# Kernel optimization log

Hardware: AMD Instinct MI355X
Metric: run time of the kernel (lower is better)

The kernel has to match this reference:

```python
import jax, jax.numpy as jnp
import numpy as np

TOP_K = 2
TEMP = 0.9
EPS = 1e-5
B, S, D, F, E = 2, 2048, 1024, 4096, 8


def setup_inputs() -> dict:
    key = jax.random.key(0)
    ks = jax.random.split(key, 4)
    scale_in = 1.0 / np.sqrt(D)
    scale_ff = 1.0 / np.sqrt(F)
    return {
        "x": jax.random.normal(ks[0], (B, S, D), jnp.float32),
        "gate_w": jax.random.normal(ks[1], (D, E), jnp.float32) * scale_in,
        "gate_b": jnp.zeros((E,), jnp.float32),
        "w1": jax.random.normal(ks[2], (E, D, F), jnp.float32) * scale_in,
        "b1": jnp.zeros((E, F), jnp.float32),
        "w2": jax.random.normal(ks[3], (E, F, D), jnp.float32) * scale_ff,
        "b2": jnp.zeros((E, D), jnp.float32),
        "ln_g": jnp.ones((D,), jnp.float32),
        "ln_b": jnp.zeros((D,), jnp.float32),
    }


def _moe_forward(x, gate_w, gate_b, w1, b1, w2, b2, ln_g, ln_b):
    # Gating: top-k masked softmax over experts
    logits = (x @ gate_w + gate_b) / TEMP                       # [B,S,E]
    topk_vals, topk_idx = jax.lax.top_k(logits, TOP_K)          # [B,S,K]
    keep = jax.nn.one_hot(topk_idx, E, dtype=jnp.bool_).any(-2)  # [B,S,E]
    masked = jnp.where(keep, logits, -jnp.inf)
    gate_probs = jax.nn.softmax(masked, axis=-1)                # [B,S,E]

    # Dense all-expert FFN (faithful to the naive original)
    h = jnp.einsum('bsd,edf->bsef', x, w1) + b1                 # [B,S,E,F]
    h = jax.nn.gelu(h, approximate=False)
    expert_out = jnp.einsum('bsef,efd->bsed', h, w2) + b2       # [B,S,E,D]

    out = jnp.einsum('bse,bsed->bsd', gate_probs, expert_out)   # combine

    # Post LayerNorm (dropout is identity in eval)
    mu = out.mean(-1, keepdims=True)
    var = out.var(-1, keepdims=True)
    out = (out - mu) / jnp.sqrt(var + EPS) * ln_g + ln_b
    return out


def reference(x, gate_w, gate_b, w1, b1, w2, b2, ln_g, ln_b):
    return _moe_forward(x, gate_w, gate_b, w1, b1, w2, b2, ln_g, ln_b)
```

## Files before the change

### kernel.cpp

```cpp
#include <hip/hip_runtime.h>
#include <stdint.h>
#include <stddef.h>

#define T_TOK 4096
#define DD    1024
#define FF    4096
#define EE    8
#define MAXROWS 9216
#define MAXTILES 72

typedef unsigned short u16;
typedef unsigned int   u32;
typedef short  sh8 __attribute__((ext_vector_type(8)));
typedef __bf16 bf8 __attribute__((ext_vector_type(8)));
typedef float  fl4 __attribute__((ext_vector_type(4)));

__device__ __forceinline__ u32 f2b_u(float f){
  u32 u = __float_as_uint(f);
  return (u + 0x7FFFu + ((u >> 16) & 1u)) >> 16;
}
__device__ __forceinline__ u16 f2b(float f){ return (u16)f2b_u(f); }
__device__ __forceinline__ u32 pack2(float a, float b){ return f2b_u(a) | (f2b_u(b) << 16); }

__device__ __forceinline__ void gl_lds16(const u16* g, u16* l){
  __builtin_amdgcn_global_load_lds(
      (const __attribute__((address_space(1))) u32*)(g),
      (__attribute__((address_space(3))) u32*)(l), 16, 0, 0);
}

__device__ __forceinline__ fl4 mfma16(sh8 a, sh8 b, fl4 c){
  return __builtin_amdgcn_mfma_f32_16x16x32_bf16(
      __builtin_bit_cast(bf8, a), __builtin_bit_cast(bf8, b), c, 0, 0, 0);
}

__device__ __forceinline__ float gelu_f(float x){
  float x2 = x * x;
  float t  = fmaf(0.07135481283f, x2, 1.5957691216f);
  float u  = x * t;
  float e  = __expf(-u);
  return x * __frcp_rn(1.0f + e);
}

__global__ __launch_bounds__(256) void k_cvt_x(const float* __restrict__ x,
                                               u16* __restrict__ xb){
  size_t i = ((size_t)blockIdx.x * 256 + threadIdx.x) * 8;
  float4 a = *(const float4*)(x + i);
  float4 b = *(const float4*)(x + i + 4);
  uint4 v;
  v.x = pack2(a.x, a.y); v.y = pack2(a.z, a.w);
  v.z = pack2(b.x, b.y); v.w = pack2(b.z, b.w);
  *(uint4*)(xb + i) = v;
}

__global__ __launch_bounds__(256) void k_gate(const float* __restrict__ x,
    const float* __restrict__ gw, const float* __restrict__ gb,
    int* __restrict__ tidx, float* __restrict__ tp, int* __restrict__ meta){
  int lane = threadIdx.x & 63;
  int t = blockIdx.x * 4 + (threadIdx.x >> 6);
  const float* xr = x + (size_t)t * DD;
  float a0=0,a1=0,a2=0,a3=0,a4=0,a5=0,a6=0,a7=0;
  #pragma unroll
  for (int i = 0; i < 16; i++){
    int d = i * 64 + lane;
    float xv = xr[d];
    const float4* g4 = (const float4*)(gw + (size_t)d * EE);
    float4 p = g4[0], q = g4[1];
    a0 += xv*p.x; a1 += xv*p.y; a2 += xv*p.z; a3 += xv*p.w;
    a4 += xv*q.x; a5 += xv*q.y; a6 += xv*q.z; a7 += xv*q.w;
  }
  #pragma unroll
  for (int off = 32; off > 0; off >>= 1){
    a0 += __shfl_xor(a0, off, 64); a1 += __shfl_xor(a1, off, 64);
    a2 += __shfl_xor(a2, off, 64); a3 += __shfl_xor(a3, off, 64);
    a4 += __shfl_xor(a4, off, 64); a5 += __shfl_xor(a5, off, 64);
    a6 += __shfl_xor(a6, off, 64); a7 += __shfl_xor(a7, off, 64);
  }
  if (lane == 0){
    float l[8] = {a0,a1,a2,a3,a4,a5,a6,a7};
    #pragma unroll
    for (int e = 0; e < 8; e++) l[e] = (l[e] + gb[e]) * (1.0f / 0.9f);
    int i1 = 0;
    #pragma unroll
    for (int e = 1; e < 8; e++) if (l[e] > l[i1]) i1 = e;
    int i2 = (i1 == 0) ? 1 : 0;
    #pragma unroll
    for (int e = 0; e < 8; e++) if (e != i1 && l[e] > l[i2]) i2 = e;
    float ex = expf(l[i2] - l[i1]);
    float inv = 1.0f / (1.0f + ex);
    tidx[2*t] = i1; tidx[2*t+1] = i2;
    tp[2*t] = inv;  tp[2*t+1] = ex * inv;
    atomicAdd(&meta[i1], 1);
    atomicAdd(&meta[i2], 1);
  }
}

__global__ __launch_bounds__(256) void k_fillscan(const int* __restrict__ tidx,
    const float* __restrict__ tp, int* __restrict__ meta,
    int* __restrict__ rowmap, float* __restrict__ rowp){
  __shared__ int sbase[EE];
  __shared__ int scur[EE];
  int tid = threadIdx.x;
  if (tid < EE) scur[tid] = 0;
  if (tid == 0){
    int rowbase = 0, total = 0;
    for (int e = 0; e < EE; e++){
      int c = meta[e];
      sbase[e] = rowbase;
      int nt = (c + 127) >> 7;
      for (int i = 0; i < nt; i++){
        meta[32 + total]  = e;
        meta[104 + total] = rowbase + i * 128;
        total++;
      }
      rowbase += nt << 7;
    }
    meta[24] = total;
  }
  __syncthreads();
  for (int t = tid; t < T_TOK; t += 256){
    #pragma unroll
    for (int k = 0; k < 2; k++){
      int e = tidx[2*t + k];
      int pos = atomicAdd(&scur[e], 1);
      int row = sbase[e] + pos;
      rowmap[row] = (t << 1) | k;
      rowp[row] = tp[2*t + k];
    }
  }
}

__global__ __launch_bounds__(256) void k_cvtw(const float* __restrict__ src,
    u16* __restrict__ dst, int R, int C){
  __shared__ float tile[64][65];
  int e = blockIdx.z;
  const float* se = src + (size_t)e * R * C;
  u16* de = dst + (size_t)e * R * C;
  int rblk = blockIdx.y * 64, cblk = blockIdx.x * 64;
  int tid = threadIdx.x;
  int lr = tid >> 4, lc = tid & 15;
  #pragma unroll
  for (int i = 0; i < 4; i++){
    int row = lr + i * 16;
    float4 v = *(const float4*)(se + (size_t)(rblk + row) * C + cblk + lc * 4);
    tile[row][lc*4+0] = v.x; tile[row][lc*4+1] = v.y;
    tile[row][lc*4+2] = v.z; tile[row][lc*4+3] = v.w;
  }
  __syncthreads();
  int c = tid >> 2, seg = tid & 3;
  u32 o[8];
  #pragma unroll
  for (int j = 0; j < 8; j++){
    float f0 = tile[seg*16 + 2*j    ][c];
    float f1 = tile[seg*16 + 2*j + 1][c];
    o[j] = pack2(f0, f1);
  }
  u16* dp = de + (size_t)(cblk + c) * R + rblk + seg * 16;
  *(uint4*)(dp)     = make_uint4(o[0], o[1], o[2], o[3]);
  *(uint4*)(dp + 8) = make_uint4(o[4], o[5], o[6], o[7]);
}

__global__ __launch_bounds__(256) void k_gemm_h(
    const u16* __restrict__ Xb, const u16* __restrict__ Wt,
    const float* __restrict__ b1, const int* __restrict__ meta,
    const int* __restrict__ rowmap, u16* __restrict__ H){
  __shared__ u16 As[128 * 64];
  __shared__ u16 Bs[128 * 64];
  int tx = blockIdx.x;
  if (tx >= meta[24]) return;
  int e = meta[32 + tx], row0 = meta[104 + tx];
  int n0 = blockIdx.y * 128;
  int tid = threadIdx.x;
  int rsub = tid >> 3;
  int sw_st = ((tid & 7) ^ (rsub & 7)) * 8;
  const u16* Be = Wt + ((size_t)e * FF + n0) * DD;
  const u16* gA[4];
  const u16* gB[4];
  #pragma unroll
  for (int j = 0; j < 4; j++){
    int row = j * 32 + rsub;
    int rm = rowmap[row0 + row];
    int tok = (rm < 0) ? 0 : (rm >> 1);
    gA[j] = Xb + (size_t)tok * DD + sw_st;
    gB[j] = Be + (size_t)row * DD + sw_st;
  }
  u16* lA = As + tid * 8;
  u16* lB = Bs + tid * 8;

  int lane = tid & 63, wv = tid >> 6;
  int wm = wv & 1, wn = wv >> 1;
  int lr = lane & 15, lq = lane >> 4;
  int sw0 = ((lq    ) ^ (lr & 7)) * 8;
  int sw1 = ((lq + 4) ^ (lr & 7)) * 8;
  const u16* pA = As + (wm * 64 + lr) * 64;
  const u16* pB = Bs + (wn * 64 + lr) * 64;

  fl4 acc[4][4];
  #pragma unroll
  for (int mi = 0; mi < 4; mi++)
    #pragma unroll
    for (int ni = 0; ni < 4; ni++) acc[mi][ni] = (fl4){0.f,0.f,0.f,0.f};

  for (int k0 = 0; k0 < DD; k0 += 64){
    #pragma unroll
    for (int j = 0; j < 4; j++){
      gl_lds16(gA[j] + k0, lA + j * 2048);
      gl_lds16(gB[j] + k0, lB + j * 2048);
    }
    __syncthreads();
    #pragma unroll
    for (int kk = 0; kk < 2; kk++){
      int sw = kk ? sw1 : sw0;
      sh8 a[4], b[4];
      #pragma unroll
      for (int mi = 0; mi < 4; mi++) a[mi] = *(const sh8*)(pA + mi * 1024 + sw);
      #pragma unroll
      for (int ni = 0; ni < 4; ni++) b[ni] = *(const sh8*)(pB + ni * 1024 + sw);
      #pragma unroll
      for (int mi = 0; mi < 4; mi++)
        #pragma unroll
        for (int ni = 0; ni < 4; ni++)
          acc[mi][ni] = mfma16(a[mi], b[ni], acc[mi][ni]);
    }
    __syncthreads();
  }

  const float* b1e = b1 + (size_t)e * FF;
  float bias[4];
  #pragma unroll
  for (int ni = 0; ni < 4; ni++) bias[ni] = b1e[n0 + wn*64 + ni*16 + lr];
  #pragma unroll
  for (int mi = 0; mi < 4; mi++){
    int grb = row0 + wm * 64 + mi * 16 + lq * 4;
    #pragma unroll
    for (int ni = 0; ni < 4; ni++){
      int gc = n0 + wn * 64 + ni * 16 + lr;
      #pragma unroll
      for (int r = 0; r < 4; r++){
        float v = acc[mi][ni][r] + bias[ni];
        H[(size_t)(grb + r) * FF + gc] = f2b(gelu_f(v));
      }
    }
  }
}

__global__ __launch_bounds__(256) void k_gemm_y(
    const u16* __restrict__ H, const u16* __restrict__ Wt,
    const float* __restrict__ b2, const int* __restrict__ meta,
    const int* __restrict__ rowmap, const float* __restrict__ rowp,
    float* __restrict__ slots){
  __shared__ u16 As[128 * 64];
  __shared__ u16 Bs[128 * 64];
  int tx = blockIdx.x;
  if (tx >= meta[24]) return;
  int e = meta[32 + tx], row0 = meta[104 + tx];
  int n0 = blockIdx.y * 128;
  int tid = threadIdx.x;
  int rsub = tid >> 3;
  int sw_st = ((tid & 7) ^ (rsub & 7)) * 8;
  const u16* Be = Wt + ((size_t)e * DD + n0) * FF;
  const u16* gA[4];
  const u16* gB[4];
  #pragma unroll
  for (int j = 0; j < 4; j++){
    int row = j * 32 + rsub;
    gA[j] = H + (size_t)(row0 + row) * FF + sw_st;
    gB[j] = Be + (size_t)row * FF + sw_st;
  }
  u16* lA = As + tid * 8;
  u16* lB = Bs + tid * 8;

  int lane = tid & 63, wv = tid >> 6;
  int wm = wv & 1, wn = wv >> 1;
  int lr = lane & 15, lq = lane >> 4;
  int sw0 = ((lq    ) ^ (lr & 7)) * 8;
  int sw1 = ((lq + 4) ^ (lr & 7)) * 8;
  const u16* pA = As + (wm * 64 + lr) * 64;
  const u16* pB = Bs + (wn * 64 + lr) * 64;

  fl4 acc[4][4];
  #pragma unroll
  for (int mi = 0; mi < 4; mi++)
    #pragma unroll
    for (int ni = 0; ni < 4; ni++) acc[mi][ni] = (fl4){0.f,0.f,0.f,0.f};

  for (int k0 = 0; k0 < FF; k0 += 64){
    #pragma unroll
    for (int j = 0; j < 4; j++){
      gl_lds16(gA[j] + k0, lA + j * 2048);
      gl_lds16(gB[j] + k0, lB + j * 2048);
    }
    __syncthreads();
    #pragma unroll
    for (int kk = 0; kk < 2; kk++){
      int sw = kk ? sw1 : sw0;
      sh8 a[4], b[4];
      #pragma unroll
      for (int mi = 0; mi < 4; mi++) a[mi] = *(const sh8*)(pA + mi * 1024 + sw);
      #pragma unroll
      for (int ni = 0; ni < 4; ni++) b[ni] = *(const sh8*)(pB + ni * 1024 + sw);
      #pragma unroll
      for (int mi = 0; mi < 4; mi++)
        #pragma unroll
        for (int ni = 0; ni < 4; ni++)
          acc[mi][ni] = mfma16(a[mi], b[ni], acc[mi][ni]);
    }
    __syncthreads();
  }

  const float* b2e = b2 + (size_t)e * DD;
  float bias[4];
  #pragma unroll
  for (int ni = 0; ni < 4; ni++) bias[ni] = b2e[n0 + wn*64 + ni*16 + lr];
  #pragma unroll
  for (int mi = 0; mi < 4; mi++){
    int grb = row0 + wm * 64 + mi * 16 + lq * 4;
    #pragma unroll
    for (int r = 0; r < 4; r++){
      int gr = grb + r;
      int sl = rowmap[gr];
      if (sl < 0) continue;
      float p = rowp[gr];
      #pragma unroll
      for (int ni = 0; ni < 4; ni++){
        int gc = n0 + wn * 64 + ni * 16 + lr;
        slots[(size_t)sl * DD + gc] = (acc[mi][ni][r] + bias[ni]) * p;
      }
    }
  }
}

__global__ __launch_bounds__(256) void k_ln(const float* __restrict__ slots,
    const float* __restrict__ lng, const float* __restrict__ lnb,
    float* __restrict__ out){
  int lane = threadIdx.x & 63;
  int t = blockIdx.x * 4 + (threadIdx.x >> 6);
  const float* s0 = slots + (size_t)(2 * t) * DD;
  const float* s1 = s0 + DD;
  float y[16];
  float sum = 0.f, sq = 0.f;
  #pragma unroll
  for (int i = 0; i < 2; i++){
    int d = lane * 8 + i * 512;
    float4 p0 = *(const float4*)(s0 + d);
    float4 p1 = *(const float4*)(s0 + d + 4);
    float4 q0 = *(const float4*)(s1 + d);
    float4 q1 = *(const float4*)(s1 + d + 4);
    y[i*8+0]=p0.x+q0.x; y[i*8+1]=p0.y+q0.y; y[i*8+2]=p0.z+q0.z; y[i*8+3]=p0.w+q0.w;
    y[i*8+4]=p1.x+q1.x; y[i*8+5]=p1.y+q1.y; y[i*8+6]=p1.z+q1.z; y[i*8+7]=p1.w+q1.w;
  }
  #pragma unroll
  for (int j = 0; j < 16; j++){ sum += y[j]; sq += y[j]*y[j]; }
  #pragma unroll
  for (int off = 32; off > 0; off >>= 1){
    sum += __shfl_xor(sum, off, 64);
    sq  += __shfl_xor(sq,  off, 64);
  }
  float mu = sum * (1.0f / DD);
  float var = sq * (1.0f / DD) - mu * mu;
  float rs = 1.0f / sqrtf(var + 1e-5f);
  #pragma unroll
  for (int i = 0; i < 2; i++){
    int d = lane * 8 + i * 512;
    float4 g0 = *(const float4*)(lng + d), g1 = *(const float4*)(lng + d + 4);
    float4 c0 = *(const float4*)(lnb + d), c1 = *(const float4*)(lnb + d + 4);
    float4 o0, o1;
    o0.x=(y[i*8+0]-mu)*rs*g0.x+c0.x; o0.y=(y[i*8+1]-mu)*rs*g0.y+c0.y;
    o0.z=(y[i*8+2]-mu)*rs*g0.z+c0.z; o0.w=(y[i*8+3]-mu)*rs*g0.w+c0.w;
    o1.x=(y[i*8+4]-mu)*rs*g1.x+c1.x; o1.y=(y[i*8+5]-mu)*rs*g1.y+c1.y;
    o1.z=(y[i*8+6]-mu)*rs*g1.z+c1.z; o1.w=(y[i*8+7]-mu)*rs*g1.w+c1.w;
    *(float4*)(out + (size_t)t * DD + d)     = o0;
    *(float4*)(out + (size_t)t * DD + d + 4) = o1;
  }
}

extern "C" void kernel_launch(void* const* d_in, const int* in_sizes, int n_in,
                              void* d_out, int out_size, void* d_ws, size_t ws_size,
                              hipStream_t stream){
  const float* x   = (const float*)d_in[0];
  const float* gw  = (const float*)d_in[1];
  const float* gb  = (const float*)d_in[2];
  const float* w1  = (const float*)d_in[3];
  const float* b1  = (const float*)d_in[4];
  const float* w2  = (const float*)d_in[5];
  const float* b2  = (const float*)d_in[6];
  const float* lng = (const float*)d_in[7];
  const float* lnb = (const float*)d_in[8];
  float* out = (float*)d_out;

  char* ws = (char*)d_ws;
  size_t off = 0;
  auto alloc = [&](size_t bytes) -> void* {
    void* p = ws + off;
    off = (off + bytes + 255) & ~(size_t)255;
    return p;
  };
  int*   meta   = (int*)  alloc(256 * 4);
  int*   rowmap = (int*)  alloc(MAXROWS * 4);
  float* rowp   = (float*)alloc(MAXROWS * 4);
  int*   tidx   = (int*)  alloc(2 * T_TOK * 4);
  float* tp     = (float*)alloc(2 * T_TOK * 4);
  u16*   Xb     = (u16*)  alloc((size_t)T_TOK * DD * 2);
  float* slots  = (float*)alloc((size_t)T_TOK * 2 * DD * 4);
  u16*   H      = (u16*)  alloc((size_t)MAXROWS * FF * 2);
  u16*   Wt     = (u16*)  alloc((size_t)EE * DD * FF * 2);
  (void)ws_size; (void)in_sizes; (void)n_in; (void)out_size;

  hipMemsetAsync(meta, 0, 64, stream);
  hipMemsetAsync(rowmap, 0xFF, MAXROWS * 4, stream);

  k_cvt_x   <<<(T_TOK * DD) / (256 * 8), 256, 0, stream>>>(x, Xb);
  k_gate    <<<T_TOK / 4, 256, 0, stream>>>(x, gw, gb, tidx, tp, meta);
  k_fillscan<<<1, 256, 0, stream>>>(tidx, tp, meta, rowmap, rowp);

  k_cvtw  <<<dim3(FF / 64, DD / 64, EE), 256, 0, stream>>>(w1, Wt, DD, FF);
  k_gemm_h<<<dim3(MAXTILES, FF / 128), 256, 0, stream>>>(Xb, Wt, b1, meta, rowmap, H);
  k_cvtw  <<<dim3(DD / 64, FF / 64, EE), 256, 0, stream>>>(w2, Wt, FF, DD);
  k_gemm_y<<<dim3(MAXTILES, DD / 128), 256, 0, stream>>>(H, Wt, b2, meta, rowmap, rowp, slots);

  k_ln    <<<T_TOK / 4, 256, 0, stream>>>(slots, lng, lnb, out);
}
```

Before: 709.8 us.

## Double-buffer LDS in both expert GEMMs and split-K the second GEMM

Both grouped GEMM kernels now use two LDS buffers, so the next K slice is loaded while MFMAs run on the current one, hiding global-load latency behind compute. The down-projection GEMM is also split along K into two halves across grid z. Partial results are combined with atomicAdd into a zero-initialised slots buffer, with the bias added only by the first half. This doubles the block count of the under-occupied second GEMM, at the cost of twice the LDS per block (64KB), an extra memset, and atomic traffic.

```diff
diff --git a/kernel.cpp b/kernel.cpp
--- a/kernel.cpp
+++ b/kernel.cpp
@@ -163,8 +163,7 @@
     const u16* __restrict__ Xb, const u16* __restrict__ Wt,
     const float* __restrict__ b1, const int* __restrict__ meta,
     const int* __restrict__ rowmap, u16* __restrict__ H){
-  __shared__ u16 As[128 * 64];
-  __shared__ u16 Bs[128 * 64];
+  __shared__ u16 A0[128*64], B0[128*64], A1[128*64], B1[128*64];
   int tx = blockIdx.x;
   if (tx >= meta[24]) return;
   int e = meta[32 + tx], row0 = meta[104 + tx];
@@ -183,16 +182,14 @@
     gA[j] = Xb + (size_t)tok * DD + sw_st;
     gB[j] = Be + (size_t)row * DD + sw_st;
   }
-  u16* lA = As + tid * 8;
-  u16* lB = Bs + tid * 8;
 
   int lane = tid & 63, wv = tid >> 6;
   int wm = wv & 1, wn = wv >> 1;
   int lr = lane & 15, lq = lane >> 4;
   int sw0 = ((lq    ) ^ (lr & 7)) * 8;
   int sw1 = ((lq + 4) ^ (lr & 7)) * 8;
-  const u16* pA = As + (wm * 64 + lr) * 64;
-  const u16* pB = Bs + (wn * 64 + lr) * 64;
+  int offA = (wm * 64 + lr) * 64;
+  int offB = (wn * 64 + lr) * 64;
 
   fl4 acc[4][4];
   #pragma unroll
@@ -200,28 +197,38 @@
     #pragma unroll
     for (int ni = 0; ni < 4; ni++) acc[mi][ni] = (fl4){0.f,0.f,0.f,0.f};
 
-  for (int k0 = 0; k0 < DD; k0 += 64){
+  auto stage = [&](int k0, u16* dA, u16* dB){
     #pragma unroll
     for (int j = 0; j < 4; j++){
-      gl_lds16(gA[j] + k0, lA + j * 2048);
-      gl_lds16(gB[j] + k0, lB + j * 2048);
-    }
-    __syncthreads();
+      gl_lds16(gA[j] + k0, dA + tid * 8 + j * 2048);
+      gl_lds16(gB[j] + k0, dB + tid * 8 + j * 2048);
+    }
+  };
+  auto compute = [&](const u16* bufA, const u16* bufB){
     #pragma unroll
     for (int kk = 0; kk < 2; kk++){
       int sw = kk ? sw1 : sw0;
       sh8 a[4], b[4];
       #pragma unroll
-      for (int mi = 0; mi < 4; mi++) a[mi] = *(const sh8*)(pA + mi * 1024 + sw);
-      #pragma unroll
-      for (int ni = 0; ni < 4; ni++) b[ni] = *(const sh8*)(pB + ni * 1024 + sw);
+      for (int mi = 0; mi < 4; mi++) a[mi] = *(const sh8*)(bufA + offA + mi * 1024 + sw);
+      #pragma unroll
+      for (int ni = 0; ni < 4; ni++) b[ni] = *(const sh8*)(bufB + offB + ni * 1024 + sw);
       #pragma unroll
       for (int mi = 0; mi < 4; mi++)
         #pragma unroll
         for (int ni = 0; ni < 4; ni++)
           acc[mi][ni] = mfma16(a[mi], b[ni], acc[mi][ni]);
     }
+  };
+
+  stage(0, A0, B0);
+  for (int k0 = 0; k0 < DD; k0 += 128){
     __syncthreads();
+    stage(k0 + 64, A1, B1);
+    compute(A0, B0);
+    __syncthreads();
+    if (k0 + 128 < DD) stage(k0 + 128, A0, B0);
+    compute(A1, B1);
   }
 
   const float* b1e = b1 + (size_t)e * FF;
@@ -248,34 +255,33 @@
     const float* __restrict__ b2, const int* __restrict__ meta,
     const int* __restrict__ rowmap, const float* __restrict__ rowp,
     float* __restrict__ slots){
-  __shared__ u16 As[128 * 64];
-  __shared__ u16 Bs[128 * 64];
+  __shared__ u16 A0[128*64], B0[128*64], A1[128*64], B1[128*64];
   int tx = blockIdx.x;
   if (tx >= meta[24]) return;
   int e = meta[32 + tx], row0 = meta[104 + tx];
   int n0 = blockIdx.y * 128;
+  int kz = blockIdx.z;
+  int kbase = kz * (FF / 2);
   int tid = threadIdx.x;
   int rsub = tid >> 3;
   int sw_st = ((tid & 7) ^ (rsub & 7)) * 8;
-  const u16* Be = Wt + ((size_t)e * DD + n0) * FF;
+  const u16* Be = Wt + ((size_t)e * DD + n0) * FF + kbase;
   const u16* gA[4];
   const u16* gB[4];
   #pragma unroll
   for (int j = 0; j < 4; j++){
     int row = j * 32 + rsub;
-    gA[j] = H + (size_t)(row0 + row) * FF + sw_st;
+    gA[j] = H + (size_t)(row0 + row) * FF + kbase + sw_st;
     gB[j] = Be + (size_t)row * FF + sw_st;
   }
-  u16* lA = As + tid * 8;
-  u16* lB = Bs + tid * 8;
 
   int lane = tid & 63, wv = tid >> 6;
   int wm = wv & 1, wn = wv >> 1;
   int lr = lane & 15, lq = lane >> 4;
   int sw0 = ((lq    ) ^ (lr & 7)) * 8;
   int sw1 = ((lq + 4) ^ (lr & 7)) * 8;
-  const u16* pA = As + (wm * 64 + lr) * 64;
-  const u16* pB = Bs + (wn * 64 + lr) * 64;
+  int offA = (wm * 64 + lr) * 64;
+  int offB = (wn * 64 + lr) * 64;
 
   fl4 acc[4][4];
   #pragma unroll
@@ -283,34 +289,46 @@
     #pragma unroll
     for (int ni = 0; ni < 4; ni++) acc[mi][ni] = (fl4){0.f,0.f,0.f,0.f};
 
-  for (int k0 = 0; k0 < FF; k0 += 64){
+  auto stage = [&](int k0, u16* dA, u16* dB){
     #pragma unroll
     for (int j = 0; j < 4; j++){
-      gl_lds16(gA[j] + k0, lA + j * 2048);
-      gl_lds16(gB[j] + k0, lB + j * 2048);
-    }
-    __syncthreads();
+      gl_lds16(gA[j] + k0, dA + tid * 8 + j * 2048);
+      gl_lds16(gB[j] + k0, dB + tid * 8 + j * 2048);
+    }
+  };
+  auto compute = [&](const u16* bufA, const u16* bufB){
     #pragma unroll
     for (int kk = 0; kk < 2; kk++){
       int sw = kk ? sw1 : sw0;
       sh8 a[4], b[4];
       #pragma unroll
-      for (int mi = 0; mi < 4; mi++) a[mi] = *(const sh8*)(pA + mi * 1024 + sw);
-      #pragma unroll
-      for (int ni = 0; ni < 4; ni++) b[ni] = *(const sh8*)(pB + ni * 1024 + sw);
+      for (int mi = 0; mi < 4; mi++) a[mi] = *(const sh8*)(bufA + offA + mi * 1024 + sw);
+      #pragma unroll
+      for (int ni = 0; ni < 4; ni++) b[ni] = *(const sh8*)(bufB + offB + ni * 1024 + sw);
       #pragma unroll
       for (int mi = 0; mi < 4; mi++)
         #pragma unroll
         for (int ni = 0; ni < 4; ni++)
           acc[mi][ni] = mfma16(a[mi], b[ni], acc[mi][ni]);
     }
+  };
+
+  const int KC = FF / 2;
+  stage(0, A0, B0);
+  for (int k0 = 0; k0 < KC; k0 += 128){
     __syncthreads();
+    stage(k0 + 64, A1, B1);
+    compute(A0, B0);
+    __syncthreads();
+    if (k0 + 128 < KC) stage(k0 + 128, A0, B0);
+    compute(A1, B1);
   }
 
   const float* b2e = b2 + (size_t)e * DD;
   float bias[4];
   #pragma unroll
-  for (int ni = 0; ni < 4; ni++) bias[ni] = b2e[n0 + wn*64 + ni*16 + lr];
+  for (int ni = 0; ni < 4; ni++)
+    bias[ni] = (kz == 0) ? b2e[n0 + wn*64 + ni*16 + lr] : 0.0f;
   #pragma unroll
   for (int mi = 0; mi < 4; mi++){
     int grb = row0 + wm * 64 + mi * 16 + lq * 4;
@@ -323,7 +341,7 @@
       #pragma unroll
       for (int ni = 0; ni < 4; ni++){
         int gc = n0 + wn * 64 + ni * 16 + lr;
-        slots[(size_t)sl * DD + gc] = (acc[mi][ni][r] + bias[ni]) * p;
+        atomicAdd(&slots[(size_t)sl * DD + gc], (acc[mi][ni][r] + bias[ni]) * p);
       }
     }
   }
@@ -407,6 +425,7 @@
 
   hipMemsetAsync(meta, 0, 64, stream);
   hipMemsetAsync(rowmap, 0xFF, MAXROWS * 4, stream);
+  hipMemsetAsync(slots, 0, (size_t)T_TOK * 2 * DD * 4, stream);
 
   k_cvt_x   <<<(T_TOK * DD) / (256 * 8), 256, 0, stream>>>(x, Xb);
   k_gate    <<<T_TOK / 4, 256, 0, stream>>>(x, gw, gb, tidx, tp, meta);
@@ -415,7 +434,7 @@
   k_cvtw  <<<dim3(FF / 64, DD / 64, EE), 256, 0, stream>>>(w1, Wt, DD, FF);
   k_gemm_h<<<dim3(MAXTILES, FF / 128), 256, 0, stream>>>(Xb, Wt, b1, meta, rowmap, H);
   k_cvtw  <<<dim3(DD / 64, FF / 64, EE), 256, 0, stream>>>(w2, Wt, FF, DD);
-  k_gemm_y<<<dim3(MAXTILES, DD / 128), 256, 0, stream>>>(H, Wt, b2, meta, rowmap, rowp, slots);
+  k_gemm_y<<<dim3(MAXTILES, DD / 128, 2), 256, 0, stream>>>(H, Wt, b2, meta, rowmap, rowp, slots);
 
   k_ln    <<<T_TOK / 4, 256, 0, stream>>>(slots, lng, lnb, out);
 }
```

New measurement: 731.9 us. 1.03x slower.
